# Performance work log

Measured on AMD Instinct MI355X. Metric: run time of the kernel, lower is better.

The kernel has to match this reference:

```python
import jax, jax.numpy as jnp
import numpy as np

TOP_K = 8
N_GROUP = 8
TOPK_GROUP = 4
ROUTED_SCALING = 2.5
NUM_EXPERTS = 256
HIDDEN = 4096
TOKENS = 16384


def setup_inputs() -> dict:
    key = jax.random.key(0)
    k1, k2 = jax.random.split(key)
    hidden_states = jax.random.normal(k1, (TOKENS, HIDDEN), dtype=jnp.float32)
    # Linear weight [num_experts, hidden]; scaled init for sane logits
    gate_w = jax.random.normal(k2, (NUM_EXPERTS, HIDDEN), dtype=jnp.float32) * (1.0 / np.sqrt(HIDDEN))
    expert_bias = jnp.zeros((NUM_EXPERTS,), dtype=jnp.float32)
    return {"hidden_states": hidden_states, "gate_w": gate_w, "expert_bias": expert_bias}


def _group_limited_topk(scores):
    # scores: [T, E]
    T, E = scores.shape
    g = scores.reshape(T, N_GROUP, E // N_GROUP)
    # sum of top-2 scores within each group -> group score [T, n_group]
    top2, _ = jax.lax.top_k(g, 2)
    group_scores = top2.sum(axis=-1)
    _, group_idx = jax.lax.top_k(group_scores, TOPK_GROUP)  # [T, topk_group]
    # group mask [T, n_group]
    group_mask = jax.nn.one_hot(group_idx, N_GROUP, dtype=scores.dtype).sum(axis=1) > 0
    score_mask = jnp.repeat(group_mask, E // N_GROUP, axis=1)  # [T, E]
    masked_scores = jnp.where(score_mask, scores, -jnp.inf)
    probs, top_indices = jax.lax.top_k(masked_scores, TOP_K)
    return probs, top_indices


def reference(hidden_states, gate_w, expert_bias):
    x = hidden_states.reshape(-1, hidden_states.shape[-1])
    logits = jnp.einsum("th,eh->te", x, gate_w).astype(jnp.float32)  # [T, E]
    scores = jax.nn.sigmoid(logits)
    scores_for_routing = scores + expert_bias[None, :]
    _, topk_idx = _group_limited_topk(scores_for_routing)  # [T, top_k]
    gathered = jnp.take_along_axis(scores, topk_idx, axis=1)  # [T, top_k]
    if TOP_K > 1:
        topk_weight = gathered / (gathered.sum(axis=-1, keepdims=True) + 1e-20)
    else:
        topk_weight = gathered
    topk_weight = topk_weight * ROUTED_SCALING
    return topk_idx, topk_weight, logits
```

## Files before the change

### kernel.cpp

```cpp
#include <hip/hip_runtime.h>
#include <math.h>

#define TOKENS  16384
#define HIDDEN  4096
#define NEXPERT 256
#define NGROUP  8
#define GSIZE   32
#define TOPKG   4
#define TOPK    8
#define RSCALE  2.5f

#define BM  64
#define BK  16
#define LDA 68
#define LDB 260

__device__ __forceinline__ float sigmoid_acc(float x) {
    return 1.0f / (1.0f + expf(-x));
}

__global__ __launch_bounds__(256, 1) __attribute__((amdgpu_waves_per_eu(1, 1)))
void moe_gate_fused(const float* __restrict__ A,
                    const float* __restrict__ B,
                    const float* __restrict__ bias,
                    float* __restrict__ out_idx,
                    float* __restrict__ out_w,
                    float* __restrict__ out_logits)
{
    __shared__ float As[2][BK * LDA];
    __shared__ float Bs[2][BK * LDB];
    __shared__ float gsum[BM][NGROUP + 1];

    const int tid = threadIdx.x;
    const int m0  = blockIdx.x * BM;

    const int ar = tid >> 2;
    const int kq = tid & 3;
    const float* Ag = A + (long)(m0 + ar) * HIDDEN + kq * 4;
    const float* Bg = B + (long)ar * HIDDEN + kq * 4;

    const int tr   = tid >> 5;
    const int tc   = tid & 31;
    const int row0 = tr * 8;
    const int c0   = tc * 4;

    float4 pa, pb0, pb1, pb2, pb3;

    pa  = *(const float4*)(Ag);
    pb0 = *(const float4*)(Bg + (long)0 * 64 * HIDDEN);
    pb1 = *(const float4*)(Bg + (long)1 * 64 * HIDDEN);
    pb2 = *(const float4*)(Bg + (long)2 * 64 * HIDDEN);
    pb3 = *(const float4*)(Bg + (long)3 * 64 * HIDDEN);

    {
        float* as = As[0];
        as[(kq * 4 + 0) * LDA + ar] = pa.x;
        as[(kq * 4 + 1) * LDA + ar] = pa.y;
        as[(kq * 4 + 2) * LDA + ar] = pa.z;
        as[(kq * 4 + 3) * LDA + ar] = pa.w;
        float* bs = Bs[0];
        float vb[4][4] = {{pb0.x,pb0.y,pb0.z,pb0.w},{pb1.x,pb1.y,pb1.z,pb1.w},
                          {pb2.x,pb2.y,pb2.z,pb2.w},{pb3.x,pb3.y,pb3.z,pb3.w}};
        #pragma unroll
        for (int p = 0; p < 4; ++p)
            #pragma unroll
            for (int j = 0; j < 4; ++j)
                bs[(kq * 4 + j) * LDB + p * 64 + ar] = vb[p][j];
    }
    __syncthreads();

    float acc[8][8] = {};

    const int NKT = HIDDEN / BK;
    for (int kt = 0; kt < NKT; ++kt) {
        const int cur = kt & 1;

        if (kt + 1 < NKT) {
            const int ko = (kt + 1) * BK;
            pa  = *(const float4*)(Ag + ko);
            pb0 = *(const float4*)(Bg + (long)0 * 64 * HIDDEN + ko);
            pb1 = *(const float4*)(Bg + (long)1 * 64 * HIDDEN + ko);
            pb2 = *(const float4*)(Bg + (long)2 * 64 * HIDDEN + ko);
            pb3 = *(const float4*)(Bg + (long)3 * 64 * HIDDEN + ko);
        }

        const float* as = As[cur];
        const float* bs = Bs[cur];
        #pragma unroll
        for (int k = 0; k < BK; ++k) {
            float4 a0 = *(const float4*)(as + k * LDA + row0);
            float4 a1 = *(const float4*)(as + k * LDA + row0 + 4);
            float4 b0 = *(const float4*)(bs + k * LDB + c0);
            float4 b1 = *(const float4*)(bs + k * LDB + 128 + c0);
            float av[8] = {a0.x, a0.y, a0.z, a0.w, a1.x, a1.y, a1.z, a1.w};
            float bv[8] = {b0.x, b0.y, b0.z, b0.w, b1.x, b1.y, b1.z, b1.w};
            #pragma unroll
            for (int i = 0; i < 8; ++i)
                #pragma unroll
                for (int j = 0; j < 8; ++j)
                    acc[i][j] = fmaf(av[i], bv[j], acc[i][j]);
        }

        if (kt + 1 < NKT) {
            float* as_w = As[cur ^ 1];
            as_w[(kq * 4 + 0) * LDA + ar] = pa.x;
            as_w[(kq * 4 + 1) * LDA + ar] = pa.y;
            as_w[(kq * 4 + 2) * LDA + ar] = pa.z;
            as_w[(kq * 4 + 3) * LDA + ar] = pa.w;
            float* bs_w = Bs[cur ^ 1];
            float vb[4][4] = {{pb0.x,pb0.y,pb0.z,pb0.w},{pb1.x,pb1.y,pb1.z,pb1.w},
                              {pb2.x,pb2.y,pb2.z,pb2.w},{pb3.x,pb3.y,pb3.z,pb3.w}};
            #pragma unroll
            for (int p = 0; p < 4; ++p)
                #pragma unroll
                for (int j = 0; j < 4; ++j)
                    bs_w[(kq * 4 + j) * LDB + p * 64 + ar] = vb[p][j];
        }
        __syncthreads();
    }

    #pragma unroll
    for (int i = 0; i < 8; ++i) {
        long row = m0 + row0 + i;
        *(float4*)(out_logits + row * NEXPERT + c0)       = make_float4(acc[i][0], acc[i][1], acc[i][2], acc[i][3]);
        *(float4*)(out_logits + row * NEXPERT + 128 + c0) = make_float4(acc[i][4], acc[i][5], acc[i][6], acc[i][7]);
    }
    __syncthreads();

    for (int task = tid; task < BM * NGROUP; task += 256) {
        const int tt = task >> 3;
        const int g  = task & 7;
        const float* lg = out_logits + (long)(m0 + tt) * NEXPERT + g * GSIZE;
        const float* bp = bias + g * GSIZE;
        float m1 = -INFINITY, m2 = -INFINITY;
        #pragma unroll
        for (int j4 = 0; j4 < GSIZE / 4; ++j4) {
            float4 l = *(const float4*)(lg + j4 * 4);
            float4 b = *(const float4*)(bp + j4 * 4);
            float vv[4] = {sigmoid_acc(l.x) + b.x, sigmoid_acc(l.y) + b.y,
                           sigmoid_acc(l.z) + b.z, sigmoid_acc(l.w) + b.w};
            #pragma unroll
            for (int c = 0; c < 4; ++c) {
                float x = vv[c];
                if (x > m1) { m2 = m1; m1 = x; }
                else if (x > m2) { m2 = x; }
            }
        }
        gsum[tt][g] = m1 + m2;
    }
    __syncthreads();

    if (tid < BM) {
        const long tok = m0 + tid;
        const float* lg = out_logits + tok * NEXPERT;

        float gs[NGROUP];
        #pragma unroll
        for (int g = 0; g < NGROUP; ++g) gs[g] = gsum[tid][g];

        unsigned selmask = 0;
        #pragma unroll
        for (int r = 0; r < TOPKG; ++r) {
            float best = -INFINITY; int bi = 0;
            #pragma unroll
            for (int g = 0; g < NGROUP; ++g) {
                bool taken = (selmask >> g) & 1u;
                if (!taken && gs[g] > best) { best = gs[g]; bi = g; }
            }
            selmask |= 1u << bi;
        }

        float rv[TOPK]; int ri[TOPK];
        #pragma unroll
        for (int k = 0; k < TOPK; ++k) { rv[k] = -INFINITY; ri[k] = 0; }

        for (int g = 0; g < NGROUP; ++g) {
            if (!((selmask >> g) & 1u)) continue;
            #pragma unroll 4
            for (int j = 0; j < GSIZE; ++j) {
                int e = g * GSIZE + j;
                float v = sigmoid_acc(lg[e]) + bias[e];
                if (v > rv[TOPK - 1]) {
                    rv[TOPK - 1] = v; ri[TOPK - 1] = e;
                    #pragma unroll
                    for (int q = TOPK - 1; q > 0; --q) {
                        if (rv[q] > rv[q - 1]) {
                            float tv = rv[q]; rv[q] = rv[q - 1]; rv[q - 1] = tv;
                            int   ti = ri[q]; ri[q] = ri[q - 1]; ri[q - 1] = ti;
                        }
                    }
                }
            }
        }

        float pv[TOPK]; float sum = 0.0f;
        #pragma unroll
        for (int k = 0; k < TOPK; ++k) { pv[k] = rv[k] - bias[ri[k]]; sum += pv[k]; }
        float denom = sum + 1e-20f;

        #pragma unroll
        for (int k = 0; k < TOPK; ++k) {
            out_idx[tok * TOPK + k] = (float)ri[k];
            out_w[tok * TOPK + k]   = pv[k] / denom * RSCALE;
        }
    }
}

extern "C" void kernel_launch(void* const* d_in, const int* in_sizes, int n_in,
                              void* d_out, int out_size, void* d_ws, size_t ws_size,
                              hipStream_t stream) {
    const float* hidden = (const float*)d_in[0];
    const float* gate_w = (const float*)d_in[1];
    const float* bias   = (const float*)d_in[2];

    float* out = (float*)d_out;
    float* out_idx    = out;
    float* out_w      = out + (long)TOKENS * TOPK;
    float* out_logits = out + (long)TOKENS * TOPK * 2;

    moe_gate_fused<<<TOKENS / BM, 256, 0, stream>>>(
        hidden, gate_w, bias, out_idx, out_w, out_logits);
}
```

Baseline: 864.8 us.

## Double threads per block to 512 with 8x4 per-thread tiles

Raises the block to 512 threads, so each thread computes an 8x4 output micro-tile instead of 8x8, and remaps the global-to-shared load assignment to match (float2 for A, two float4 for B per thread). Launch bounds change to allow two waves per EU. The goal is more resident waves to hide memory and LDS latency. The cost is a lower FMA-to-LDS-read ratio per thread, because A fragments are now reused across only 4 columns.

```diff
diff --git a/kernel.cpp b/kernel.cpp
--- a/kernel.cpp
+++ b/kernel.cpp
@@ -10,16 +10,17 @@
 #define TOPK    8
 #define RSCALE  2.5f
 
-#define BM  64
-#define BK  16
-#define LDA 68
-#define LDB 260
+#define BM   64
+#define BK   16
+#define LDA  68
+#define LDB  260
+#define NTHR 512
 
 __device__ __forceinline__ float sigmoid_acc(float x) {
     return 1.0f / (1.0f + expf(-x));
 }
 
-__global__ __launch_bounds__(256, 1) __attribute__((amdgpu_waves_per_eu(1, 1)))
+__global__ __launch_bounds__(NTHR, 2) __attribute__((amdgpu_waves_per_eu(2, 2)))
 void moe_gate_fused(const float* __restrict__ A,
                     const float* __restrict__ B,
                     const float* __restrict__ bias,
@@ -34,42 +35,43 @@
     const int tid = threadIdx.x;
     const int m0  = blockIdx.x * BM;
 
-    const int ar = tid >> 2;
-    const int kq = tid & 3;
-    const float* Ag = A + (long)(m0 + ar) * HIDDEN + kq * 4;
-    const float* Bg = B + (long)ar * HIDDEN + kq * 4;
-
-    const int tr   = tid >> 5;
-    const int tc   = tid & 31;
+    const int ar_a = tid >> 3;
+    const int kh   = tid & 7;
+    const int ar_b = tid >> 1;
+    const int q0   = (tid & 1) * 2;
+
+    const float* Ag = A + (long)(m0 + ar_a) * HIDDEN + kh * 2;
+    const float* Bg = B + (long)ar_b * HIDDEN + q0 * 4;
+
+    const int tr   = tid >> 6;
+    const int tc   = tid & 63;
     const int row0 = tr * 8;
     const int c0   = tc * 4;
 
-    float4 pa, pb0, pb1, pb2, pb3;
-
-    pa  = *(const float4*)(Ag);
-    pb0 = *(const float4*)(Bg + (long)0 * 64 * HIDDEN);
-    pb1 = *(const float4*)(Bg + (long)1 * 64 * HIDDEN);
-    pb2 = *(const float4*)(Bg + (long)2 * 64 * HIDDEN);
-    pb3 = *(const float4*)(Bg + (long)3 * 64 * HIDDEN);
+    float2 qa;
+    float4 pb0, pb1;
+
+    qa  = *(const float2*)(Ag);
+    pb0 = *(const float4*)(Bg);
+    pb1 = *(const float4*)(Bg + 4);
 
     {
         float* as = As[0];
-        as[(kq * 4 + 0) * LDA + ar] = pa.x;
-        as[(kq * 4 + 1) * LDA + ar] = pa.y;
-        as[(kq * 4 + 2) * LDA + ar] = pa.z;
-        as[(kq * 4 + 3) * LDA + ar] = pa.w;
+        as[(kh * 2 + 0) * LDA + ar_a] = qa.x;
+        as[(kh * 2 + 1) * LDA + ar_a] = qa.y;
         float* bs = Bs[0];
-        float vb[4][4] = {{pb0.x,pb0.y,pb0.z,pb0.w},{pb1.x,pb1.y,pb1.z,pb1.w},
-                          {pb2.x,pb2.y,pb2.z,pb2.w},{pb3.x,pb3.y,pb3.z,pb3.w}};
-        #pragma unroll
-        for (int p = 0; p < 4; ++p)
-            #pragma unroll
-            for (int j = 0; j < 4; ++j)
-                bs[(kq * 4 + j) * LDB + p * 64 + ar] = vb[p][j];
+        bs[(q0 * 4 + 0) * LDB + ar_b] = pb0.x;
+        bs[(q0 * 4 + 1) * LDB + ar_b] = pb0.y;
+        bs[(q0 * 4 + 2) * LDB + ar_b] = pb0.z;
+        bs[(q0 * 4 + 3) * LDB + ar_b] = pb0.w;
+        bs[(q0 * 4 + 4) * LDB + ar_b] = pb1.x;
+        bs[(q0 * 4 + 5) * LDB + ar_b] = pb1.y;
+        bs[(q0 * 4 + 6) * LDB + ar_b] = pb1.z;
+        bs[(q0 * 4 + 7) * LDB + ar_b] = pb1.w;
     }
     __syncthreads();
 
-    float acc[8][8] = {};
+    float acc[8][4] = {};
 
     const int NKT = HIDDEN / BK;
     for (int kt = 0; kt < NKT; ++kt) {
@@ -77,11 +79,9 @@
 
         if (kt + 1 < NKT) {
             const int ko = (kt + 1) * BK;
-            pa  = *(const float4*)(Ag + ko);
-            pb0 = *(const float4*)(Bg + (long)0 * 64 * HIDDEN + ko);
-            pb1 = *(const float4*)(Bg + (long)1 * 64 * HIDDEN + ko);
-            pb2 = *(const float4*)(Bg + (long)2 * 64 * HIDDEN + ko);
-            pb3 = *(const float4*)(Bg + (long)3 * 64 * HIDDEN + ko);
+            qa  = *(const float2*)(Ag + ko);
+            pb0 = *(const float4*)(Bg + ko);
+            pb1 = *(const float4*)(Bg + ko + 4);
         }
 
         const float* as = As[cur];
@@ -91,30 +91,28 @@
             float4 a0 = *(const float4*)(as + k * LDA + row0);
             float4 a1 = *(const float4*)(as + k * LDA + row0 + 4);
             float4 b0 = *(const float4*)(bs + k * LDB + c0);
-            float4 b1 = *(const float4*)(bs + k * LDB + 128 + c0);
             float av[8] = {a0.x, a0.y, a0.z, a0.w, a1.x, a1.y, a1.z, a1.w};
-            float bv[8] = {b0.x, b0.y, b0.z, b0.w, b1.x, b1.y, b1.z, b1.w};
+            float bv[4] = {b0.x, b0.y, b0.z, b0.w};
             #pragma unroll
             for (int i = 0; i < 8; ++i)
                 #pragma unroll
-                for (int j = 0; j < 8; ++j)
+                for (int j = 0; j < 4; ++j)
                     acc[i][j] = fmaf(av[i], bv[j], acc[i][j]);
         }
 
         if (kt + 1 < NKT) {
             float* as_w = As[cur ^ 1];
-            as_w[(kq * 4 + 0) * LDA + ar] = pa.x;
-            as_w[(kq * 4 + 1) * LDA + ar] = pa.y;
-            as_w[(kq * 4 + 2) * LDA + ar] = pa.z;
-            as_w[(kq * 4 + 3) * LDA + ar] = pa.w;
+            as_w[(kh * 2 + 0) * LDA + ar_a] = qa.x;
+            as_w[(kh * 2 + 1) * LDA + ar_a] = qa.y;
             float* bs_w = Bs[cur ^ 1];
-            float vb[4][4] = {{pb0.x,pb0.y,pb0.z,pb0.w},{pb1.x,pb1.y,pb1.z,pb1.w},
-                              {pb2.x,pb2.y,pb2.z,pb2.w},{pb3.x,pb3.y,pb3.z,pb3.w}};
-            #pragma unroll
-            for (int p = 0; p < 4; ++p)
-                #pragma unroll
-                for (int j = 0; j < 4; ++j)
-                    bs_w[(kq * 4 + j) * LDB + p * 64 + ar] = vb[p][j];
+            bs_w[(q0 * 4 + 0) * LDB + ar_b] = pb0.x;
+            bs_w[(q0 * 4 + 1) * LDB + ar_b] = pb0.y;
+            bs_w[(q0 * 4 + 2) * LDB + ar_b] = pb0.z;
+            bs_w[(q0 * 4 + 3) * LDB + ar_b] = pb0.w;
+            bs_w[(q0 * 4 + 4) * LDB + ar_b] = pb1.x;
+            bs_w[(q0 * 4 + 5) * LDB + ar_b] = pb1.y;
+            bs_w[(q0 * 4 + 6) * LDB + ar_b] = pb1.z;
+            bs_w[(q0 * 4 + 7) * LDB + ar_b] = pb1.w;
         }
         __syncthreads();
     }
@@ -122,12 +120,12 @@
     #pragma unroll
     for (int i = 0; i < 8; ++i) {
         long row = m0 + row0 + i;
-        *(float4*)(out_logits + row * NEXPERT + c0)       = make_float4(acc[i][0], acc[i][1], acc[i][2], acc[i][3]);
-        *(float4*)(out_logits + row * NEXPERT + 128 + c0) = make_float4(acc[i][4], acc[i][5], acc[i][6], acc[i][7]);
+        *(float4*)(out_logits + row * NEXPERT + c0) =
+            make_float4(acc[i][0], acc[i][1], acc[i][2], acc[i][3]);
     }
     __syncthreads();
 
-    for (int task = tid; task < BM * NGROUP; task += 256) {
+    for (int task = tid; task < BM * NGROUP; task += NTHR) {
         const int tt = task >> 3;
         const int g  = task & 7;
         const float* lg = out_logits + (long)(m0 + tt) * NEXPERT + g * GSIZE;
@@ -218,6 +216,6 @@
     float* out_w      = out + (long)TOKENS * TOPK;
     float* out_logits = out + (long)TOKENS * TOPK * 2;
 
-    moe_gate_fused<<<TOKENS / BM, 256, 0, stream>>>(
+    moe_gate_fused<<<TOKENS / BM, NTHR, 0, stream>>>(
         hidden, gate_w, bias, out_idx, out_w, out_logits);
 }
```

Result: faster. 742.5 us (-14.1%).
